# Kernel optimization log

Measured on AMD Instinct MI355X. Metric: run time of the kernel, lower is better.

Reference implementation:

```python
import jax, jax.numpy as jnp
import numpy as np


def setup_inputs() -> dict:
    key = jax.random.key(0)
    B, S, K = 4, 4096, 64
    attn_scores = jax.random.normal(key, (B, S, S), dtype=jnp.float32)
    return {"attn_scores": attn_scores, "k": K}


def reference(attn_scores, k):
    # attn_scores: [B, S, S]; k: python int
    B, S, _ = attn_scores.shape
    # topk over last dim -> indices [B, S, k]
    _, idx = jax.lax.top_k(attn_scores, k)
    # torch.scatter(newmask, 1, idx, zeros): newmask[b, idx[b,s,j], j] = False
    # for s in range(S), j in range(k) (only first k columns are written).
    mask = jnp.ones((B, S, S), dtype=bool)
    b = jnp.arange(B)[:, None, None]      # [B,1,1]
    j = jnp.arange(k)[None, None, :]      # [1,1,k]
    mask = mask.at[b, idx, j].set(False)  # scatter False along row dim
    # triangular overwrite: for i in range(k+1): mask[:, i, i+1:] = True
    rows = jnp.arange(S)[:, None]         # [S,1]
    cols = jnp.arange(S)[None, :]         # [1,S]
    tri = (rows < (k + 1)) & (cols > rows)  # [S,S]
    mask = jnp.where(tri[None, :, :], True, mask)
    return mask[:, None, :, :]            # [B,1,S,S]
```

## Files before the change

### kernel.cpp

```cpp
#include <hip/hip_runtime.h>
#include <stdint.h>

#define S_DIM 4096
#define K_TOP 64
#define THREADS 256
#define EPT 16
#define CAND_CAP 256

__global__ __launch_bounds__(256) void fill_ones_kernel(int4* __restrict__ out, int n4) {
    int i = blockIdx.x * blockDim.x + threadIdx.x;
    const int stride = gridDim.x * blockDim.x;
    const int4 v = make_int4(1, 1, 1, 1);
    for (; i < n4; i += stride) out[i] = v;
}

__device__ __forceinline__ unsigned long long shfl_xor_u64(unsigned long long v, int m) {
    uint32_t lo = (uint32_t)v, hi = (uint32_t)(v >> 32);
    lo = __shfl_xor(lo, m, 64);
    hi = __shfl_xor(hi, m, 64);
    return ((unsigned long long)hi << 32) | lo;
}

__global__ __launch_bounds__(256) void topk_scatter_kernel(const float* __restrict__ scores,
                                                           int* __restrict__ out) {
    const int row  = blockIdx.x;
    const int b    = row >> 12;
    const int t    = threadIdx.x;
    const int lane = t & 63;
    const int wid  = t >> 6;

    __shared__ uint32_t sh_w16[4];
    __shared__ unsigned long long cand[CAND_CAP];
    __shared__ uint32_t sh_count;
    __shared__ unsigned long long sh_wbest[4];
    __shared__ unsigned long long sh_best;

    const float4* rowp = (const float4*)(scores + (size_t)row * S_DIM);
    uint32_t key[EPT];
    #pragma unroll
    for (int i = 0; i < 4; ++i) {
        float4 v = rowp[i * THREADS + t];
        float f[4] = {v.x, v.y, v.z, v.w};
        #pragma unroll
        for (int c = 0; c < 4; ++c) {
            uint32_t ub = __float_as_uint(f[c]);
            key[i * 4 + c] = (ub & 0x80000000u) ? ~ub : (ub | 0x80000000u);
        }
    }

    if (t == 0) sh_count = 0u;

    uint32_t mx = key[0];
    #pragma unroll
    for (int i = 1; i < EPT; ++i) mx = max(mx, key[i]);

    uint32_t x = mx;
    #pragma unroll
    for (int k = 2; k <= 64; k <<= 1) {
        #pragma unroll
        for (int j = k >> 1; j > 0; j >>= 1) {
            uint32_t v = __shfl_xor(x, j, 64);
            bool keepMin = (((lane & j) == 0) == ((lane & k) == 0));
            x = keepMin ? min(x, v) : max(x, v);
        }
    }
    uint32_t w16 = __shfl(x, 48, 64);
    if (lane == 0) sh_w16[wid] = w16;
    __syncthreads();

    const uint32_t Tc = min(min(sh_w16[0], sh_w16[1]), min(sh_w16[2], sh_w16[3]));

    #pragma unroll
    for (int i = 0; i < EPT; ++i) {
        if (key[i] >= Tc) {
            uint32_t idx = (((uint32_t)(i >> 2) * THREADS + (uint32_t)t) << 2) | (uint32_t)(i & 3);
            uint32_t pos = atomicAdd(&sh_count, 1u);
            if (pos < CAND_CAP) {
                cand[pos] = ((unsigned long long)key[i] << 32) | (uint32_t)(~idx);
            }
        }
    }
    __syncthreads();
    const uint32_t m = sh_count;

    if (m <= CAND_CAP) {
        if ((uint32_t)t < m) {
            unsigned long long me = cand[t];
            uint32_t rank = 0;
            for (uint32_t i = 0; i < m; ++i) rank += (cand[i] > me) ? 1u : 0u;
            if (rank < K_TOP) {
                uint32_t idx = ~(uint32_t)me;
                if (idx >= rank) {
                    out[(size_t)b * ((size_t)S_DIM * S_DIM) + (size_t)idx * S_DIM + rank] = 0;
                }
            }
        }
        return;
    }

    uint32_t used = 0u;
    for (int r = 0; r < K_TOP; ++r) {
        unsigned long long best = 0ull;
        #pragma unroll
        for (int i = 0; i < EPT; ++i) {
            if (!(used & (1u << i))) {
                uint32_t idx = (((uint32_t)(i >> 2) * THREADS + (uint32_t)t) << 2) | (uint32_t)(i & 3);
                unsigned long long ck = ((unsigned long long)key[i] << 32) | (uint32_t)(~idx);
                if (ck > best) best = ck;
            }
        }
        #pragma unroll
        for (int off = 32; off > 0; off >>= 1) {
            unsigned long long o = shfl_xor_u64(best, off);
            if (o > best) best = o;
        }
        if (lane == 0) sh_wbest[wid] = best;
        __syncthreads();
        if (t == 0) {
            unsigned long long bb = sh_wbest[0];
            for (int w = 1; w < 4; ++w) if (sh_wbest[w] > bb) bb = sh_wbest[w];
            sh_best = bb;
        }
        __syncthreads();
        const unsigned long long gb = sh_best;
        #pragma unroll
        for (int i = 0; i < EPT; ++i) {
            uint32_t idx = (((uint32_t)(i >> 2) * THREADS + (uint32_t)t) << 2) | (uint32_t)(i & 3);
            unsigned long long ck = ((unsigned long long)key[i] << 32) | (uint32_t)(~idx);
            if (ck == gb) {
                used |= (1u << i);
                uint32_t oidx = ~(uint32_t)gb;
                if (oidx >= (uint32_t)r) {
                    out[(size_t)b * ((size_t)S_DIM * S_DIM) + (size_t)oidx * S_DIM + r] = 0;
                }
            }
        }
        __syncthreads();
    }
}

extern "C" void kernel_launch(void* const* d_in, const int* in_sizes, int n_in,
                              void* d_out, int out_size, void* d_ws, size_t ws_size,
                              hipStream_t stream) {
    const float* scores = (const float*)d_in[0];
    int* out = (int*)d_out;

    const int n4 = out_size / 4;
    hipLaunchKernelGGL(fill_ones_kernel, dim3(2048), dim3(THREADS), 0, stream,
                       (int4*)out, n4);

    const int B = in_sizes[0] / (S_DIM * S_DIM);
    hipLaunchKernelGGL(topk_scatter_kernel, dim3(B * S_DIM), dim3(THREADS), 0, stream,
                       scores, out);
}
```

Measured before the change: 456.5 us.

## Fuse bulk ones-fill into topk kernel, prefill only first 64 columns

The separate full-output fill of ones is replaced by a small prefill kernel that writes only the first 64 columns of each row. The topk kernel now writes ones to columns 64 and beyond for its own row while the score loads are in flight. Scatter writes only touch columns below 64, so the prefill kernel must finish first to keep those zeros from being overwritten. This removes a separate full pass over the output and overlaps the bulk stores with the top-k compute.

```diff
diff --git a/kernel.cpp b/kernel.cpp
--- a/kernel.cpp
+++ b/kernel.cpp
@@ -7,11 +7,12 @@
 #define EPT 16
 #define CAND_CAP 256
 
-__global__ __launch_bounds__(256) void fill_ones_kernel(int4* __restrict__ out, int n4) {
-    int i = blockIdx.x * blockDim.x + threadIdx.x;
-    const int stride = gridDim.x * blockDim.x;
-    const int4 v = make_int4(1, 1, 1, 1);
-    for (; i < n4; i += stride) out[i] = v;
+__global__ __launch_bounds__(256) void prefill_edge_kernel(int4* __restrict__ out, int nrows) {
+    int L = blockIdx.x * blockDim.x + threadIdx.x;
+    if (L >= nrows * 16) return;
+    int row = L >> 4;
+    int q   = L & 15;
+    out[(size_t)row * (S_DIM / 4) + q] = make_int4(1, 1, 1, 1);
 }
 
 __device__ __forceinline__ unsigned long long shfl_xor_u64(unsigned long long v, int m) {
@@ -36,15 +37,25 @@
     __shared__ unsigned long long sh_best;
 
     const float4* rowp = (const float4*)(scores + (size_t)row * S_DIM);
+    float4 v0 = rowp[0 * THREADS + t];
+    float4 v1 = rowp[1 * THREADS + t];
+    float4 v2 = rowp[2 * THREADS + t];
+    float4 v3 = rowp[3 * THREADS + t];
+
+    {
+        int4* orow = (int4*)(out + (size_t)row * S_DIM);
+        const int4 ones = make_int4(1, 1, 1, 1);
+        for (int j = 16 + t; j < S_DIM / 4; j += THREADS) orow[j] = ones;
+    }
+
     uint32_t key[EPT];
-    #pragma unroll
-    for (int i = 0; i < 4; ++i) {
-        float4 v = rowp[i * THREADS + t];
-        float f[4] = {v.x, v.y, v.z, v.w};
+    {
+        float f[EPT] = {v0.x, v0.y, v0.z, v0.w, v1.x, v1.y, v1.z, v1.w,
+                        v2.x, v2.y, v2.z, v2.w, v3.x, v3.y, v3.z, v3.w};
         #pragma unroll
-        for (int c = 0; c < 4; ++c) {
-            uint32_t ub = __float_as_uint(f[c]);
-            key[i * 4 + c] = (ub & 0x80000000u) ? ~ub : (ub | 0x80000000u);
+        for (int i = 0; i < EPT; ++i) {
+            uint32_t ub = __float_as_uint(f[i]);
+            key[i] = (ub & 0x80000000u) ? ~ub : (ub | 0x80000000u);
         }
     }
 
@@ -145,11 +156,13 @@
     const float* scores = (const float*)d_in[0];
     int* out = (int*)d_out;
 
-    const int n4 = out_size / 4;
-    hipLaunchKernelGGL(fill_ones_kernel, dim3(2048), dim3(THREADS), 0, stream,
-                       (int4*)out, n4);
+    const int B = in_sizes[0] / (S_DIM * S_DIM);
+    const int nrows = B * S_DIM;
 
-    const int B = in_sizes[0] / (S_DIM * S_DIM);
-    hipLaunchKernelGGL(topk_scatter_kernel, dim3(B * S_DIM), dim3(THREADS), 0, stream,
+    const int prefill_threads = nrows * 16;
+    hipLaunchKernelGGL(prefill_edge_kernel, dim3((prefill_threads + THREADS - 1) / THREADS),
+                       dim3(THREADS), 0, stream, (int4*)out, nrows);
+
+    hipLaunchKernelGGL(topk_scatter_kernel, dim3(nrows), dim3(THREADS), 0, stream,
                        scores, out);
 }
```

New measurement: 435.3 us. -4.7%, faster.
